# Optimization experiments

Measured on AMD Instinct MI355X. Metric: run time of the kernel, lower is better.

Reference implementation:

```python
import jax, jax.numpy as jnp
import numpy as np

B, N, IN_DIM, OUT_DIM = 8, 2048, 128, 128
NEG_SLOPE = 0.2

def setup_inputs() -> dict:
    key = jax.random.key(0)
    k1, k2, k3, k4 = jax.random.split(key, 4)
    x = jax.random.normal(k1, (B, N, IN_DIM), dtype=jnp.float32)
    adj = jax.random.randint(k2, (N, N), 0, 2, dtype=jnp.int32)
    # nn.Linear weight init scale ~ 1/sqrt(fan_in)
    W = jax.random.normal(k3, (IN_DIM, OUT_DIM), dtype=jnp.float32) / np.sqrt(IN_DIM)
    a_vec = jax.random.normal(k4, (2 * OUT_DIM,), dtype=jnp.float32) / np.sqrt(2 * OUT_DIM)
    return {"x": x, "adj": adj, "W": W, "a_vec": a_vec}

def reference(x, adj, W, a_vec):
    # h = x @ W : [b, n, d]
    h = jnp.einsum("bni,io->bno", x, W)
    # Algebraic decomposition of a([h_i, h_j]) = a1.h_i + a2.h_j
    a1, a2 = a_vec[:OUT_DIM], a_vec[OUT_DIM:]
    s_i = h @ a1  # [b, n] score contribution from source node i
    s_j = h @ a2  # [b, n] score contribution from target node j
    e = s_i[:, :, None] + s_j[:, None, :]  # [b, n, n]
    e = jnp.where(e >= 0, e, NEG_SLOPE * e)  # leaky_relu(0.2)
    mask = (adj > 0)[None, :, :]  # [1, n, n] broadcast over batch
    e = jnp.where(mask, e, -jnp.inf)
    alpha = jax.nn.softmax(e, axis=-1)  # [b, n, n]
    out = jnp.einsum("bnm,bmd->bnd", alpha, h)  # [b, n, d]
    return out, alpha
```

## Files before the change

kernel.cpp:

```cpp
#include <hip/hip_runtime.h>
#include <hip/hip_bf16.h>
#include <cstdint>
#include <cstddef>

constexpr int Bn = 8;
constexpr int Nn = 2048;
constexpr int Dn = 128;

typedef __bf16 bf16x8 __attribute__((ext_vector_type(8)));
typedef float f32x4 __attribute__((ext_vector_type(4)));

__global__ __launch_bounds__(256) void gat_k1(
    const float* __restrict__ x, const float* __restrict__ W,
    const float* __restrict__ a_vec,
    __bf16* __restrict__ hT, float* __restrict__ s1, float* __restrict__ s2) {
  __shared__ __align__(16) float Wl[64 * 144];
  __shared__ __align__(16) float xL[32 * 132];

  const int t = threadIdx.x;
  const int r0 = blockIdx.x * 32;
  const int b = r0 >> 11;
  const int n0 = r0 & (Nn - 1);
  const int rp = (t >> 4) << 1;
  const int c0 = (t & 15) << 3;
  const int c0p = c0 + ((c0 >> 5) << 2);

  float acc[2][8];
#pragma unroll
  for (int r = 0; r < 2; ++r)
#pragma unroll
    for (int c = 0; c < 8; ++c) acc[r][c] = 0.f;

#pragma unroll
  for (int it = 0; it < 4; ++it) {
    int idx = t + (it << 8);
    int rr = idx >> 5, kc = (idx & 31) << 2;
    *(float4*)(xL + rr * 132 + kc) = *(const float4*)(x + (size_t)(r0 + rr) * Dn + kc);
  }

  for (int ph = 0; ph < 2; ++ph) {
    if (ph) __syncthreads();
#pragma unroll
    for (int it = 0; it < 8; ++it) {
      int idx = t + (it << 8);
      int kk = idx >> 5, c4 = (idx & 31) << 2;
      int dsto = kk * 144 + c4 + ((c4 >> 5) << 2);
      *(float4*)(Wl + dsto) = *(const float4*)(W + (size_t)((ph << 6) + kk) * Dn + c4);
    }
    __syncthreads();
    const float* xrow = xL + rp * 132 + (ph << 6);
    for (int k = 0; k < 64; ++k) {
      float xa0 = xrow[k];
      float xa1 = xrow[132 + k];
      float4 w0 = *(const float4*)(Wl + k * 144 + c0p);
      float4 w1 = *(const float4*)(Wl + k * 144 + c0p + 4);
      float ws[8] = {w0.x, w0.y, w0.z, w0.w, w1.x, w1.y, w1.z, w1.w};
#pragma unroll
      for (int c = 0; c < 8; ++c) {
        acc[0][c] = fmaf(xa0, ws[c], acc[0][c]);
        acc[1][c] = fmaf(xa1, ws[c], acc[1][c]);
      }
    }
  }

  float q1[2] = {0.f, 0.f}, q2[2] = {0.f, 0.f};
#pragma unroll
  for (int c = 0; c < 8; ++c) {
    float a1c = a_vec[c0 + c];
    float a2c = a_vec[Dn + c0 + c];
    q1[0] = fmaf(acc[0][c], a1c, q1[0]);
    q1[1] = fmaf(acc[1][c], a1c, q1[1]);
    q2[0] = fmaf(acc[0][c], a2c, q2[0]);
    q2[1] = fmaf(acc[1][c], a2c, q2[1]);
  }
#pragma unroll
  for (int d = 1; d < 16; d <<= 1) {
    q1[0] += __shfl_xor(q1[0], d);
    q1[1] += __shfl_xor(q1[1], d);
    q2[0] += __shfl_xor(q2[0], d);
    q2[1] += __shfl_xor(q2[1], d);
  }
  if ((t & 15) == 0) {
    s1[b * Nn + n0 + rp] = q1[0];
    s1[b * Nn + n0 + rp + 1] = q1[1];
    s2[b * Nn + n0 + rp] = q2[0];
    s2[b * Nn + n0 + rp + 1] = q2[1];
  }

#pragma unroll
  for (int c = 0; c < 8; ++c) {
    union { __bf16 h[2]; uint32_t u; } pk;
    pk.h[0] = (__bf16)acc[0][c];
    pk.h[1] = (__bf16)acc[1][c];
    *(uint32_t*)(hT + (size_t)(b * Dn + c0 + c) * Nn + n0 + rp) = pk.u;
  }
}

__global__ __launch_bounds__(512, 8) void gat_k2(
    const int* __restrict__ adj, const __bf16* __restrict__ hT,
    const float* __restrict__ s1, const float* __restrict__ s2,
    float* __restrict__ out, float* __restrict__ alpha) {
  __shared__ __align__(16) float sj[Nn];
  __shared__ float siv[16], invl[16];
  __shared__ __align__(16) __bf16 Pl[2][16 * 128];

  const int t = threadIdx.x;
  const int b = blockIdx.x >> 7;
  const int i0 = (blockIdx.x & 127) << 4;
  const int w = t >> 6, lane = t & 63;
  const int row = t >> 5;
  const int jl = (t & 31) << 2;
  const int q16 = lane >> 4, m16 = lane & 15;
  const int d0 = w << 4;
  const __bf16* __restrict__ hTb = hT + (size_t)b * Dn * Nn;

  *(float4*)(sj + (t << 2)) = *(const float4*)(s2 + b * Nn + (t << 2));
  if (t < 16) siv[t] = s1[b * Nn + i0 + t];
  __syncthreads();

  const int i = i0 + row;
  const int* __restrict__ adjrow = adj + (size_t)i * Nn;
  const float si = siv[row];

  float l = 0.f;
  uint32_t mb0 = 0, mb1 = 0;
#pragma unroll
  for (int k = 0; k < 16; ++k) {
    int j = (k << 7) + jl;
    int4 am = *(const int4*)(adjrow + j);
    float4 sv = *(const float4*)(sj + j);
    float e0 = si + sv.x; e0 = fmaxf(e0, 0.2f * e0);
    float e1 = si + sv.y; e1 = fmaxf(e1, 0.2f * e1);
    float e2 = si + sv.z; e2 = fmaxf(e2, 0.2f * e2);
    float e3 = si + sv.w; e3 = fmaxf(e3, 0.2f * e3);
    l += (am.x > 0) ? __expf(e0) : 0.f;
    l += (am.y > 0) ? __expf(e1) : 0.f;
    l += (am.z > 0) ? __expf(e2) : 0.f;
    l += (am.w > 0) ? __expf(e3) : 0.f;
    uint32_t mbt = (am.x > 0 ? 1u : 0u) | (am.y > 0 ? 2u : 0u) |
                   (am.z > 0 ? 4u : 0u) | (am.w > 0 ? 8u : 0u);
    if (k < 8) mb0 |= mbt << (k << 2);
    else       mb1 |= mbt << ((k & 7) << 2);
  }
  l += __shfl_xor(l, 1);
  l += __shfl_xor(l, 2);
  l += __shfl_xor(l, 4);
  l += __shfl_xor(l, 8);
  l += __shfl_xor(l, 16);
  if ((t & 31) == 0) invl[row] = 1.f / l;
  __syncthreads();
  const float il = invl[row];

  f32x4 acc = {0.f, 0.f, 0.f, 0.f};
  float* __restrict__ arow = alpha + ((size_t)(b * Nn + i) << 11);

  const __bf16* __restrict__ bp = hTb + (size_t)(d0 + m16) * Nn + (q16 << 3);
  const int swz = (m16 & 7) << 4;

  auto alpha_phase = [&](int k) {
    int j = (k << 7) + jl;
    float4 sv = *(const float4*)(sj + j);
    uint32_t mw = (k & 8) ? mb1 : mb0;
    int sh = (k & 7) << 2;
    float e0 = si + sv.x; e0 = fmaxf(e0, 0.2f * e0);
    float e1 = si + sv.y; e1 = fmaxf(e1, 0.2f * e1);
    float e2 = si + sv.z; e2 = fmaxf(e2, 0.2f * e2);
    float e3 = si + sv.w; e3 = fmaxf(e3, 0.2f * e3);
    float a0 = ((mw >> (sh + 0)) & 1u) ? __expf(e0) * il : 0.f;
    float a1 = ((mw >> (sh + 1)) & 1u) ? __expf(e1) * il : 0.f;
    float a2 = ((mw >> (sh + 2)) & 1u) ? __expf(e2) * il : 0.f;
    float a3 = ((mw >> (sh + 3)) & 1u) ? __expf(e3) * il : 0.f;
    f32x4 av = {a0, a1, a2, a3};
    __builtin_nontemporal_store(av, (f32x4*)(arow + j));
    union { __bf16 h[4]; uint2 u2; } pk;
    pk.h[0] = (__bf16)a0; pk.h[1] = (__bf16)a1;
    pk.h[2] = (__bf16)a2; pk.h[3] = (__bf16)a3;
    *(uint2*)((char*)(&Pl[k & 1][0]) + (row << 8) +
              (((jl << 1)) ^ ((row & 7) << 4))) = pk.u2;
  };

  auto mfma_win = [&](int parity, bf16x8 c0, bf16x8 c1, bf16x8 c2, bf16x8 c3) {
    const char* plb = (const char*)(&Pl[parity][0]) + (m16 << 8);
    bf16x8 a0 = *(const bf16x8*)(plb + (((0 << 6) + (q16 << 4)) ^ swz));
    bf16x8 a1 = *(const bf16x8*)(plb + (((1 << 6) + (q16 << 4)) ^ swz));
    bf16x8 a2 = *(const bf16x8*)(plb + (((2 << 6) + (q16 << 4)) ^ swz));
    bf16x8 a3 = *(const bf16x8*)(plb + (((3 << 6) + (q16 << 4)) ^ swz));
    acc = __builtin_amdgcn_mfma_f32_16x16x32_bf16(a0, c0, acc, 0, 0, 0);
    acc = __builtin_amdgcn_mfma_f32_16x16x32_bf16(a1, c1, acc, 0, 0, 0);
    acc = __builtin_amdgcn_mfma_f32_16x16x32_bf16(a2, c2, acc, 0, 0, 0);
    acc = __builtin_amdgcn_mfma_f32_16x16x32_bf16(a3, c3, acc, 0, 0, 0);
  };

  alpha_phase(0);
  asm volatile("s_waitcnt lgkmcnt(0)\n\ts_barrier" ::: "memory");

#pragma unroll
  for (int jt = 0; jt < 16; ++jt) {
    const __bf16* cp = bp + (jt << 7);
    bf16x8 c0 = *(const bf16x8*)(cp);
    bf16x8 c1 = *(const bf16x8*)(cp + 32);
    bf16x8 c2 = *(const bf16x8*)(cp + 64);
    bf16x8 c3 = *(const bf16x8*)(cp + 96);
    __builtin_amdgcn_sched_barrier(0);
    if (jt < 15) alpha_phase(jt + 1);
    mfma_win(jt & 1, c0, c1, c2, c3);
    if (jt < 15)
      asm volatile("s_waitcnt lgkmcnt(0)\n\ts_barrier" ::: "memory");
  }

  int d = d0 + m16;
#pragma unroll
  for (int r = 0; r < 4; ++r) {
    int irow = i0 + (q16 << 2) + r;
    out[((size_t)(b * Nn + irow) << 7) + d] = acc[r];
  }
}

extern "C" void kernel_launch(void* const* d_in, const int* in_sizes, int n_in,
                              void* d_out, int out_size, void* d_ws, size_t ws_size,
                              hipStream_t stream) {
  const float* x = (const float*)d_in[0];
  const int* adj = (const int*)d_in[1];
  const float* W = (const float*)d_in[2];
  const float* a_vec = (const float*)d_in[3];

  float* out = (float*)d_out;
  float* alpha = out + (size_t)Bn * Nn * Dn;

  char* ws = (char*)d_ws;
  __bf16* hT = (__bf16*)ws;
  float* s1 = (float*)(ws + (size_t)Bn * Dn * Nn * 2);
  float* s2 = s1 + (size_t)Bn * Nn;

  gat_k1<<<512, 256, 0, stream>>>(x, W, a_vec, hT, s1, s2);
  gat_k2<<<1024, 512, 0, stream>>>(adj, hT, s1, s2, out, alpha);
}
```

Baseline: 232.0 us.

## Split attention kernel over j across waves with register-resident MFMA A operands

Restructures the attention kernel so each of four waves owns a quarter of the neighbor dimension for all 16 rows and all 128 output columns. Probabilities are computed directly in the MFMA A-operand layout, so the LDS staging buffer and per-tile barriers are gone, and the adjacency is read again instead of being kept as bitmasks. Partial accumulators are reduced across waves through LDS at the end, and output is written with vectorized nontemporal stores. Block size drops from 512 to 256 threads. The trade-off is a second adj read, eight accumulator tiles per wave that raise register pressure, and an extra cross-wave reduction.

```diff
diff --git a/kernel.cpp b/kernel.cpp
--- a/kernel.cpp
+++ b/kernel.cpp
@@ -96,123 +96,135 @@
   }
 }
 
-__global__ __launch_bounds__(512, 8) void gat_k2(
+__global__ __launch_bounds__(256, 4) void gat_k2(
     const int* __restrict__ adj, const __bf16* __restrict__ hT,
     const float* __restrict__ s1, const float* __restrict__ s2,
     float* __restrict__ out, float* __restrict__ alpha) {
-  __shared__ __align__(16) float sj[Nn];
-  __shared__ float siv[16], invl[16];
-  __shared__ __align__(16) __bf16 Pl[2][16 * 128];
+  __shared__ __align__(16) float accL[4 * 16 * 128];
+  __shared__ float lq[4][16];
+  float* const sj = accL;
 
   const int t = threadIdx.x;
   const int b = blockIdx.x >> 7;
   const int i0 = (blockIdx.x & 127) << 4;
-  const int w = t >> 6, lane = t & 63;
-  const int row = t >> 5;
-  const int jl = (t & 31) << 2;
+  const int jq = t >> 6, lane = t & 63;
   const int q16 = lane >> 4, m16 = lane & 15;
-  const int d0 = w << 4;
-  const __bf16* __restrict__ hTb = hT + (size_t)b * Dn * Nn;
-
-  *(float4*)(sj + (t << 2)) = *(const float4*)(s2 + b * Nn + (t << 2));
-  if (t < 16) siv[t] = s1[b * Nn + i0 + t];
-  __syncthreads();
-
-  const int i = i0 + row;
-  const int* __restrict__ adjrow = adj + (size_t)i * Nn;
-  const float si = siv[row];
+  const int jo = (jq << 9) + (q16 << 3);
+
+  *(float4*)(sj + (t << 3)) = *(const float4*)(s2 + b * Nn + (t << 3));
+  *(float4*)(sj + (t << 3) + 4) = *(const float4*)(s2 + b * Nn + (t << 3) + 4);
+  asm volatile("s_waitcnt lgkmcnt(0)\n\ts_barrier" ::: "memory");
+
+  const int i = i0 + m16;
+  const float si = s1[b * Nn + i];
+  const int* __restrict__ adjrow = adj + (size_t)i * Nn + jo;
+  const float* __restrict__ sjl = sj + jo;
 
   float l = 0.f;
-  uint32_t mb0 = 0, mb1 = 0;
-#pragma unroll
-  for (int k = 0; k < 16; ++k) {
-    int j = (k << 7) + jl;
-    int4 am = *(const int4*)(adjrow + j);
-    float4 sv = *(const float4*)(sj + j);
-    float e0 = si + sv.x; e0 = fmaxf(e0, 0.2f * e0);
-    float e1 = si + sv.y; e1 = fmaxf(e1, 0.2f * e1);
-    float e2 = si + sv.z; e2 = fmaxf(e2, 0.2f * e2);
-    float e3 = si + sv.w; e3 = fmaxf(e3, 0.2f * e3);
-    l += (am.x > 0) ? __expf(e0) : 0.f;
-    l += (am.y > 0) ? __expf(e1) : 0.f;
-    l += (am.z > 0) ? __expf(e2) : 0.f;
-    l += (am.w > 0) ? __expf(e3) : 0.f;
-    uint32_t mbt = (am.x > 0 ? 1u : 0u) | (am.y > 0 ? 2u : 0u) |
-                   (am.z > 0 ? 4u : 0u) | (am.w > 0 ? 8u : 0u);
-    if (k < 8) mb0 |= mbt << (k << 2);
-    else       mb1 |= mbt << ((k & 7) << 2);
-  }
-  l += __shfl_xor(l, 1);
-  l += __shfl_xor(l, 2);
-  l += __shfl_xor(l, 4);
-  l += __shfl_xor(l, 8);
+#pragma unroll 4
+  for (int jt = 0; jt < 16; ++jt) {
+    int o = jt << 5;
+    int4 am0 = *(const int4*)(adjrow + o);
+    int4 am1 = *(const int4*)(adjrow + o + 4);
+    float4 v0 = *(const float4*)(sjl + o);
+    float4 v1 = *(const float4*)(sjl + o + 4);
+    float e0 = si + v0.x; e0 = fmaxf(e0, 0.2f * e0);
+    float e1 = si + v0.y; e1 = fmaxf(e1, 0.2f * e1);
+    float e2 = si + v0.z; e2 = fmaxf(e2, 0.2f * e2);
+    float e3 = si + v0.w; e3 = fmaxf(e3, 0.2f * e3);
+    float e4 = si + v1.x; e4 = fmaxf(e4, 0.2f * e4);
+    float e5 = si + v1.y; e5 = fmaxf(e5, 0.2f * e5);
+    float e6 = si + v1.z; e6 = fmaxf(e6, 0.2f * e6);
+    float e7 = si + v1.w; e7 = fmaxf(e7, 0.2f * e7);
+    l += (am0.x > 0) ? __expf(e0) : 0.f;
+    l += (am0.y > 0) ? __expf(e1) : 0.f;
+    l += (am0.z > 0) ? __expf(e2) : 0.f;
+    l += (am0.w > 0) ? __expf(e3) : 0.f;
+    l += (am1.x > 0) ? __expf(e4) : 0.f;
+    l += (am1.y > 0) ? __expf(e5) : 0.f;
+    l += (am1.z > 0) ? __expf(e6) : 0.f;
+    l += (am1.w > 0) ? __expf(e7) : 0.f;
+  }
   l += __shfl_xor(l, 16);
-  if ((t & 31) == 0) invl[row] = 1.f / l;
-  __syncthreads();
-  const float il = invl[row];
-
-  f32x4 acc = {0.f, 0.f, 0.f, 0.f};
-  float* __restrict__ arow = alpha + ((size_t)(b * Nn + i) << 11);
-
-  const __bf16* __restrict__ bp = hTb + (size_t)(d0 + m16) * Nn + (q16 << 3);
-  const int swz = (m16 & 7) << 4;
-
-  auto alpha_phase = [&](int k) {
-    int j = (k << 7) + jl;
-    float4 sv = *(const float4*)(sj + j);
-    uint32_t mw = (k & 8) ? mb1 : mb0;
-    int sh = (k & 7) << 2;
-    float e0 = si + sv.x; e0 = fmaxf(e0, 0.2f * e0);
-    float e1 = si + sv.y; e1 = fmaxf(e1, 0.2f * e1);
-    float e2 = si + sv.z; e2 = fmaxf(e2, 0.2f * e2);
-    float e3 = si + sv.w; e3 = fmaxf(e3, 0.2f * e3);
-    float a0 = ((mw >> (sh + 0)) & 1u) ? __expf(e0) * il : 0.f;
-    float a1 = ((mw >> (sh + 1)) & 1u) ? __expf(e1) * il : 0.f;
-    float a2 = ((mw >> (sh + 2)) & 1u) ? __expf(e2) * il : 0.f;
-    float a3 = ((mw >> (sh + 3)) & 1u) ? __expf(e3) * il : 0.f;
-    f32x4 av = {a0, a1, a2, a3};
-    __builtin_nontemporal_store(av, (f32x4*)(arow + j));
-    union { __bf16 h[4]; uint2 u2; } pk;
-    pk.h[0] = (__bf16)a0; pk.h[1] = (__bf16)a1;
-    pk.h[2] = (__bf16)a2; pk.h[3] = (__bf16)a3;
-    *(uint2*)((char*)(&Pl[k & 1][0]) + (row << 8) +
-              (((jl << 1)) ^ ((row & 7) << 4))) = pk.u2;
-  };
-
-  auto mfma_win = [&](int parity, bf16x8 c0, bf16x8 c1, bf16x8 c2, bf16x8 c3) {
-    const char* plb = (const char*)(&Pl[parity][0]) + (m16 << 8);
-    bf16x8 a0 = *(const bf16x8*)(plb + (((0 << 6) + (q16 << 4)) ^ swz));
-    bf16x8 a1 = *(const bf16x8*)(plb + (((1 << 6) + (q16 << 4)) ^ swz));
-    bf16x8 a2 = *(const bf16x8*)(plb + (((2 << 6) + (q16 << 4)) ^ swz));
-    bf16x8 a3 = *(const bf16x8*)(plb + (((3 << 6) + (q16 << 4)) ^ swz));
-    acc = __builtin_amdgcn_mfma_f32_16x16x32_bf16(a0, c0, acc, 0, 0, 0);
-    acc = __builtin_amdgcn_mfma_f32_16x16x32_bf16(a1, c1, acc, 0, 0, 0);
-    acc = __builtin_amdgcn_mfma_f32_16x16x32_bf16(a2, c2, acc, 0, 0, 0);
-    acc = __builtin_amdgcn_mfma_f32_16x16x32_bf16(a3, c3, acc, 0, 0, 0);
-  };
-
-  alpha_phase(0);
-  asm volatile("s_waitcnt lgkmcnt(0)\n\ts_barrier" ::: "memory");
-
-#pragma unroll
+  l += __shfl_xor(l, 32);
+  if (q16 == 0) lq[jq][m16] = l;
+  asm volatile("s_waitcnt lgkmcnt(0)\n\ts_barrier" ::: "memory");
+  const float il = 1.f / (lq[0][m16] + lq[1][m16] + lq[2][m16] + lq[3][m16]);
+
+  f32x4 acc0 = {0.f, 0.f, 0.f, 0.f}, acc1 = {0.f, 0.f, 0.f, 0.f};
+  f32x4 acc2 = {0.f, 0.f, 0.f, 0.f}, acc3 = {0.f, 0.f, 0.f, 0.f};
+  f32x4 acc4 = {0.f, 0.f, 0.f, 0.f}, acc5 = {0.f, 0.f, 0.f, 0.f};
+  f32x4 acc6 = {0.f, 0.f, 0.f, 0.f}, acc7 = {0.f, 0.f, 0.f, 0.f};
+  float* __restrict__ arow = alpha + ((size_t)(b * Nn + i) << 11) + jo;
+  const __bf16* __restrict__ hrow = hT + (size_t)b * Dn * Nn + (size_t)m16 * Nn + jo;
+
+#pragma unroll 2
   for (int jt = 0; jt < 16; ++jt) {
-    const __bf16* cp = bp + (jt << 7);
-    bf16x8 c0 = *(const bf16x8*)(cp);
-    bf16x8 c1 = *(const bf16x8*)(cp + 32);
-    bf16x8 c2 = *(const bf16x8*)(cp + 64);
-    bf16x8 c3 = *(const bf16x8*)(cp + 96);
-    __builtin_amdgcn_sched_barrier(0);
-    if (jt < 15) alpha_phase(jt + 1);
-    mfma_win(jt & 1, c0, c1, c2, c3);
-    if (jt < 15)
-      asm volatile("s_waitcnt lgkmcnt(0)\n\ts_barrier" ::: "memory");
-  }
-
-  int d = d0 + m16;
-#pragma unroll
-  for (int r = 0; r < 4; ++r) {
-    int irow = i0 + (q16 << 2) + r;
-    out[((size_t)(b * Nn + irow) << 7) + d] = acc[r];
+    int o = jt << 5;
+    int4 am0 = *(const int4*)(adjrow + o);
+    int4 am1 = *(const int4*)(adjrow + o + 4);
+    float4 v0 = *(const float4*)(sjl + o);
+    float4 v1 = *(const float4*)(sjl + o + 4);
+    float e0 = si + v0.x; e0 = fmaxf(e0, 0.2f * e0);
+    float e1 = si + v0.y; e1 = fmaxf(e1, 0.2f * e1);
+    float e2 = si + v0.z; e2 = fmaxf(e2, 0.2f * e2);
+    float e3 = si + v0.w; e3 = fmaxf(e3, 0.2f * e3);
+    float e4 = si + v1.x; e4 = fmaxf(e4, 0.2f * e4);
+    float e5 = si + v1.y; e5 = fmaxf(e5, 0.2f * e5);
+    float e6 = si + v1.z; e6 = fmaxf(e6, 0.2f * e6);
+    float e7 = si + v1.w; e7 = fmaxf(e7, 0.2f * e7);
+    float a0 = (am0.x > 0) ? __expf(e0) * il : 0.f;
+    float a1 = (am0.y > 0) ? __expf(e1) * il : 0.f;
+    float a2 = (am0.z > 0) ? __expf(e2) * il : 0.f;
+    float a3 = (am0.w > 0) ? __expf(e3) * il : 0.f;
+    float a4 = (am1.x > 0) ? __expf(e4) * il : 0.f;
+    float a5 = (am1.y > 0) ? __expf(e5) * il : 0.f;
+    float a6 = (am1.z > 0) ? __expf(e6) * il : 0.f;
+    float a7 = (am1.w > 0) ? __expf(e7) * il : 0.f;
+    f32x4 w0 = {a0, a1, a2, a3};
+    f32x4 w1 = {a4, a5, a6, a7};
+    __builtin_nontemporal_store(w0, (f32x4*)(arow + o));
+    __builtin_nontemporal_store(w1, (f32x4*)(arow + o + 4));
+    bf16x8 af;
+    af[0] = (__bf16)a0; af[1] = (__bf16)a1;
+    af[2] = (__bf16)a2; af[3] = (__bf16)a3;
+    af[4] = (__bf16)a4; af[5] = (__bf16)a5;
+    af[6] = (__bf16)a6; af[7] = (__bf16)a7;
+    const __bf16* hp = hrow + o;
+#define MF(DT, A)                                                            \
+  {                                                                          \
+    bf16x8 bv = *(const bf16x8*)(hp + (size_t)(DT) * (16 * Nn));             \
+    A = __builtin_amdgcn_mfma_f32_16x16x32_bf16(af, bv, A, 0, 0, 0);         \
+  }
+    MF(0, acc0) MF(1, acc1) MF(2, acc2) MF(3, acc3)
+    MF(4, acc4) MF(5, acc5) MF(6, acc6) MF(7, acc7)
+#undef MF
+  }
+
+  asm volatile("s_waitcnt lgkmcnt(0)\n\ts_barrier" ::: "memory");
+#define WR(DT, A)                                                            \
+  {                                                                          \
+    _Pragma("unroll")                                                        \
+    for (int r = 0; r < 4; ++r)                                              \
+      accL[(jq << 11) + (((q16 << 2) + r) << 7) + ((DT) << 4) + m16] = A[r]; \
+  }
+  WR(0, acc0) WR(1, acc1) WR(2, acc2) WR(3, acc3)
+  WR(4, acc4) WR(5, acc5) WR(6, acc6) WR(7, acc7)
+#undef WR
+  asm volatile("s_waitcnt lgkmcnt(0)\n\ts_barrier" ::: "memory");
+  {
+    const int row = t >> 4, dc = (t & 15) << 3;
+    const float* p = accL + (row << 7) + dc;
+    f32x4 u0 = *(const f32x4*)(p);
+    f32x4 u1 = *(const f32x4*)(p + 4);
+#pragma unroll
+    for (int q = 1; q < 4; ++q) {
+      u0 += *(const f32x4*)(p + (q << 11));
+      u1 += *(const f32x4*)(p + (q << 11) + 4);
+    }
+    float* op = out + ((size_t)(b * Nn + i0 + row) << 7) + dc;
+    __builtin_nontemporal_store(u0, (f32x4*)op);
+    __builtin_nontemporal_store(u1, (f32x4*)(op + 4));
   }
 }
 
@@ -233,5 +245,5 @@
   float* s2 = s1 + (size_t)Bn * Nn;
 
   gat_k1<<<512, 256, 0, stream>>>(x, W, a_vec, hT, s1, s2);
-  gat_k2<<<1024, 512, 0, stream>>>(adj, hT, s1, s2, out, alpha);
+  gat_k2<<<1024, 256, 0, stream>>>(adj, hT, s1, s2, out, alpha);
 }
```

After: 246.7 us. 1.06x slower.
